# Performance work log

Hardware: AMD Instinct MI355X
Metric: run time of the kernel (lower is better)

Reference implementation:

```python
import jax, jax.numpy as jnp
import numpy as np

T_TASKS = 16      # num_tasks
N = 65536         # points per task (equal n per task -> r = 1 in the scatter)
NOISE = 100.0     # diagonal noise added at lag 0 of diagonal kernel blocks


def setup_inputs() -> dict:
    key = jax.random.key(0)
    k1_key, y_key = jax.random.split(key)
    # k1[i0, i1] : first row of the circulant kernel block for task pair (i0, i1)
    k1 = jax.random.normal(k1_key, (T_TASKS, T_TASKS, N), dtype=jnp.float32) * 0.01
    idx = jnp.arange(T_TASKS)
    k1 = k1.at[idx, idx, 0].add(NOISE)  # k1[0] += noise on diagonal blocks
    y = jax.random.normal(y_key, (T_TASKS, N), dtype=jnp.float32)
    return {"k1": k1, "y": y}


def _block_inverse(lams):
    """Sequential Schur-complement recursion from _InverseLogDetCache.

    lams: (T, T, N) complex eigenvalue vectors; only upper triangle (i0<=i1) used.
    Returns A: (T, T, N) complex (per-frequency inverse blocks), logdet (real scalar).
    """
    logdet = jnp.sum(jnp.log(jnp.abs(lams[0, 0])))
    A = (1.0 / lams[0, 0])[None, None, :]              # (1, 1, N)
    for l in range(1, lams.shape[0]):                   # loop over tasks (small, fixed)
        B = lams[:l, l, :]                              # (l, N)
        Tm = jnp.einsum('ikn,kn->in', A, B)             # T = A @ B per frequency
        M = jnp.sum(B.conj() * Tm, axis=0)              # (N,)
        S = lams[l, l] - M                              # Schur complement
        logdet = logdet + jnp.sum(jnp.log(jnp.abs(S)))
        Sinv = 1.0 / S
        P = Tm * Sinv                                   # (l, N)
        # C = P T^H + A  (r = 1 => meshgrid scatter is elementwise add of A)
        C = A + P[:, None, :] * Tm[None, :, :].conj()   # (l, l, N)
        ur = jnp.concatenate([C, -P[:, None, :]], axis=1)                     # (l, l+1, N)
        br = jnp.concatenate([-P.conj()[None, :, :], Sinv[None, None, :]], axis=1)  # (1, l+1, N)
        A = jnp.concatenate([ur, br], axis=0)           # (l+1, l+1, N)
    return A, logdet


def reference(k1, y):
    # lam = sqrt(n) * ortho-FFT(k1) == plain FFT(k1)
    lams = jnp.fft.fft(k1, axis=-1)                     # (T, T, N) complex64
    A, logdet = _block_inverse(lams)
    yt = jnp.fft.fft(y, axis=-1, norm='ortho')          # ytilde, (T, N) complex64
    quad = jnp.real(jnp.einsum('in,ijn,jn->', yt.conj(), A, yt))  # yt^H A yt
    out = jnp.concatenate([A.real.ravel(), A.imag.ravel(),
                           jnp.stack([logdet, quad]).astype(jnp.float32)])
    return out
```

## Files before the change

### kernel.cpp

```cpp
#include <hip/hip_runtime.h>
#include <hip/hip_fp16.h>


#define TT 16
#define NF 65536
#define NPAIR 136
#define NROWS 152
#define NHALF 32768

static const size_t AIMAG  = 16777216;
static const size_t OUT_LD = 33554432;
static const size_t OUT_QD = 33554433;

typedef float2 c32;

__device__ __forceinline__ c32 cmul(c32 a, c32 b) { return make_float2(a.x*b.x - a.y*b.y, a.x*b.y + a.y*b.x); }
__device__ __forceinline__ c32 cadd(c32 a, c32 b) { return make_float2(a.x + b.x, a.y + b.y); }
__device__ __forceinline__ c32 csub(c32 a, c32 b) { return make_float2(a.x - b.x, a.y - b.y); }

__constant__ c32 W16[16] = {
  { 1.0f, 0.0f}, { 0.92387953f,-0.38268343f}, { 0.70710678f,-0.70710678f}, { 0.38268343f,-0.92387953f},
  { 0.0f,-1.0f}, {-0.38268343f,-0.92387953f}, {-0.70710678f,-0.70710678f}, {-0.92387953f,-0.38268343f},
  {-1.0f, 0.0f}, {-0.92387953f, 0.38268343f}, {-0.70710678f, 0.70710678f}, {-0.38268343f, 0.92387953f},
  { 0.0f, 1.0f}, { 0.38268343f, 0.92387953f}, { 0.70710678f, 0.70710678f}, { 0.92387953f, 0.38268343f}
};

__device__ __forceinline__ void dft4(c32 a0, c32 a1, c32 a2, c32 a3,
                                     c32& c0, c32& c1, c32& c2, c32& c3) {
  c32 s0 = cadd(a0, a2), s1 = csub(a0, a2);
  c32 s2 = cadd(a1, a3), s3 = csub(a1, a3);
  c0 = cadd(s0, s2);
  c2 = csub(s0, s2);
  c1 = make_float2(s1.x + s3.y, s1.y - s3.x);
  c3 = make_float2(s1.x - s3.y, s1.y + s3.x);
}

__device__ __forceinline__ void dft16(c32 v[16]) {
  c32 t[16];
  #pragma unroll
  for (int p = 0; p < 4; ++p) {
    c32 c0, c1, c2, c3;
    dft4(v[p], v[p+4], v[p+8], v[p+12], c0, c1, c2, c3);
    t[4*p+0] = c0;
    t[4*p+1] = cmul(c1, W16[p]);
    t[4*p+2] = cmul(c2, W16[(2*p) & 15]);
    t[4*p+3] = cmul(c3, W16[(3*p) & 15]);
  }
  #pragma unroll
  for (int q = 0; q < 4; ++q) {
    c32 c0, c1, c2, c3;
    dft4(t[q], t[q+4], t[q+8], t[q+12], c0, c1, c2, c3);
    v[q+0]  = c0;
    v[q+4]  = c1;
    v[q+8]  = c2;
    v[q+12] = c3;
  }
}

__global__ __launch_bounds__(256) void fftA(const float* __restrict__ k1,
                                            const float* __restrict__ y,
                                            c32* __restrict__ out) {
  __shared__ c32 buf[16][258];
  const int t = threadIdx.x;
  const int c = t & 15;
  const int w = t >> 4;
  const int n2 = (blockIdx.x << 4) + c;
  const int row = blockIdx.y;
  const float* src;
  float scale = 1.0f;
  if (row < NPAIR) {
    int i = 0, rem = row;
    while (rem >= TT - i) { rem -= TT - i; ++i; }
    int j = i + rem;
    src = k1 + (size_t)(i * TT + j) * NF;
  } else {
    src = y + (size_t)(row - NPAIR) * NF;
    scale = 1.0f / 256.0f;
  }
  c32 v[16];
  #pragma unroll
  for (int i = 0; i < 16; ++i)
    v[i] = make_float2(src[(w + 16*i) * 256 + n2] * scale, 0.0f);
  dft16(v);
  {
    float sa, ca;
    __sincosf(-6.2831853071795865f * (float)w / 256.0f, &sa, &ca);
    c32 w1 = make_float2(ca, sa), wj = w1;
    #pragma unroll
    for (int j = 1; j < 16; ++j) { v[j] = cmul(v[j], wj); wj = cmul(wj, w1); }
  }
  #pragma unroll
  for (int j = 0; j < 16; ++j) buf[c][16*w + j] = v[j];
  __syncthreads();
  c32 u[16];
  #pragma unroll
  for (int i = 0; i < 16; ++i) u[i] = buf[c][w + 16*i];
  dft16(u);
  float sa, ca;
  __sincosf(-6.2831853071795865f * (float)(n2 * w) / 65536.0f, &sa, &ca);
  c32 tw = make_float2(ca, sa);
  __sincosf(-6.2831853071795865f * (float)n2 / 4096.0f, &sa, &ca);
  c32 st = make_float2(ca, sa);
  c32* dst = out + (size_t)row * NF + n2;
  #pragma unroll
  for (int j = 0; j < 16; ++j) {
    dst[(size_t)(w + 16*j) << 8] = cmul(u[j], tw);
    tw = cmul(tw, st);
  }
}

__global__ __launch_bounds__(256) void fftB(const c32* __restrict__ in,
                                            c32* __restrict__ out) {
  __shared__ c32 buf[16][258];
  const int t = threadIdx.x;
  const int c = t & 15;
  const int w = t >> 4;
  const int c0 = blockIdx.x << 4;
  const int row = blockIdx.y;
  const c32* src = in + (size_t)row * NF + ((size_t)c0 << 8);
  #pragma unroll
  for (int it = 0; it < 16; ++it) buf[it][t] = src[(it << 8) + t];
  __syncthreads();
  c32 v[16];
  #pragma unroll
  for (int i = 0; i < 16; ++i) v[i] = buf[c][w + 16*i];
  dft16(v);
  {
    float sa, ca;
    __sincosf(-6.2831853071795865f * (float)w / 256.0f, &sa, &ca);
    c32 w1 = make_float2(ca, sa), wj = w1;
    #pragma unroll
    for (int j = 1; j < 16; ++j) { v[j] = cmul(v[j], wj); wj = cmul(wj, w1); }
  }
  __syncthreads();
  #pragma unroll
  for (int j = 0; j < 16; ++j) buf[c][16*w + j] = v[j];
  __syncthreads();
  c32 u[16];
  #pragma unroll
  for (int i = 0; i < 16; ++i) u[i] = buf[c][w + 16*i];
  dft16(u);
  c32* dst = out + (size_t)row * NF + c0 + c;
  #pragma unroll
  for (int j = 0; j < 16; ++j) {
    int k2 = w + 16*j;
    if (k2 <= 128) dst[(size_t)k2 << 8] = u[j];
  }
}

__global__ void init_out(float* __restrict__ out) {
  if (threadIdx.x == 0 && blockIdx.x == 0) {
    out[OUT_LD] = 0.0f;
    out[OUT_QD] = 0.0f;
  }
}

__global__ __launch_bounds__(256) void invert_write(const c32* __restrict__ spec,
                                                    float* __restrict__ out) {
  __shared__ union {
    struct {
      __half2 lam[NPAIR][16];
      c32 yts[16][17];
      float4 tmb[16][17];
    } rec;
    float plane[16][260];
  } sh;
  __shared__ float redl[4], redq[4];

  const int nwg  = gridDim.x;
  const int orig = blockIdx.x;
  const int xcd  = orig & 7;
  const int pos  = orig >> 3;
  const int qq   = nwg >> 3, rm = nwg & 7;
  const int chunk = (xcd < rm ? xcd * (qq + 1) : rm * (qq + 1) + (xcd - rm) * qq) + pos;

  const int t  = threadIdx.x;
  const int fi = t >> 4;
  const int r  = t & 15;
  const int f0 = chunk << 4;
  const int f  = f0 + fi;

  for (int idx = t; idx < NPAIR * 16; idx += 256) {
    int rowi = idx >> 4, ff = idx & 15;
    c32 val = spec[(size_t)rowi * NF + f0 + ff];
    sh.rec.lam[rowi][ff] = __float22half2_rn(val);
  }
  for (int idx = NPAIR * 16 + t; idx < NROWS * 16; idx += 256) {
    int rowi = idx >> 4, ff = idx & 15;
    sh.rec.yts[ff][rowi - NPAIR] = spec[(size_t)rowi * NF + f0 + ff];
  }
  __syncthreads();

  const int rowoff = (r * (31 - r)) >> 1;

  float Ar[16], Ai[16];
  #pragma unroll
  for (int k = 0; k < 16; ++k) { Ar[k] = 0.0f; Ai[k] = 0.0f; }

  c32 l00 = __half22float2(sh.rec.lam[0][fi]);
  float m00 = l00.x*l00.x + l00.y*l00.y;
  float im00 = 1.0f / m00;
  float ld = 0.5f * __logf(m00);
  bool r0 = (r == 0);
  Ar[0] = r0 ?  l00.x * im00 : 0.0f;
  Ai[0] = r0 ? -l00.y * im00 : 0.0f;

  #pragma unroll
  for (int l = 1; l < TT; ++l) {
    float tr = 0.0f, ti = 0.0f;
    #pragma unroll
    for (int k = 0; k < l; ++k) {
      c32 B = __half22float2(sh.rec.lam[((k * (31 - k)) >> 1) + l][fi]);
      tr += Ar[k]*B.x - Ai[k]*B.y;
      ti += Ar[k]*B.y + Ai[k]*B.x;
    }
    c32 Bo = __half22float2(sh.rec.lam[rowoff + l][fi]);
    float cbr = Bo.x*tr + Bo.y*ti;
    float cbi = Bo.x*ti - Bo.y*tr;
    sh.rec.tmb[fi][r] = make_float4(tr, ti, cbr, cbi);

    float tjr[TT], tji[TT];
    float mr = 0.0f, mi = 0.0f;
    #pragma unroll
    for (int j = 0; j < l; ++j) {
      float4 q = sh.rec.tmb[fi][j];
      tjr[j] = q.x; tji[j] = q.y;
      mr += q.z;    mi += q.w;
    }

    c32 ll = __half22float2(sh.rec.lam[((l * (31 - l)) >> 1) + l][fi]);
    float Sr = ll.x - mr, Si = ll.y - mi;
    float s2 = Sr*Sr + Si*Si;
    ld += 0.5f * __logf(s2);
    float is2 = 1.0f / s2;
    float vr =  Sr * is2;
    float vi = -Si * is2;
    float pr = tr*vr - ti*vi;
    float pi = tr*vi + ti*vr;

    bool diag = (r == l);
    float cr = diag ? -vr : pr;
    float ci = diag ?  vi : pi;
    float m  = diag ? 0.0f : 1.0f;

    #pragma unroll
    for (int j = 0; j < l; ++j) {
      Ar[j] = m*Ar[j] + cr*tjr[j] + ci*tji[j];
      Ai[j] = m*Ai[j] + ci*tjr[j] - cr*tji[j];
    }
    Ar[l] = diag ? vr : -pr;
    Ai[l] = diag ? vi : -pi;
  }

  float w = (f == 0 || f == NHALF) ? 1.0f : (f < NHALF ? 2.0f : 0.0f);

  float sr = 0.0f, si = 0.0f;
  #pragma unroll
  for (int j = 0; j < 16; ++j) {
    c32 yj = sh.rec.yts[fi][j];
    sr += Ar[j]*yj.x - Ai[j]*yj.y;
    si += Ar[j]*yj.y + Ai[j]*yj.x;
  }
  c32 yr = sh.rec.yts[fi][r];
  float qd = (yr.x*sr + yr.y*si) * w;
  float lw = r0 ? ld * w : 0.0f;

  #pragma unroll
  for (int d = 1; d < 64; d <<= 1) {
    lw += __shfl_xor(lw, d, 64);
    qd += __shfl_xor(qd, d, 64);
  }
  if ((t & 63) == 0) { redl[t >> 6] = lw; redq[t >> 6] = qd; }
  __syncthreads();
  if (t == 0) {
    atomicAdd(out + OUT_LD, redl[0] + redl[1] + redl[2] + redl[3]);
    atomicAdd(out + OUT_QD, redq[0] + redq[1] + redq[2] + redq[3]);
  }

  const int lf = t & 15;
  const int cl = t >> 4;
  const int fL = f0 + lf;
  const bool dir_ok = (fL <= NHALF);
  const bool mir_ok = (fL > 0 && fL < NHALF);
  const size_t fD = (size_t)fL;
  const size_t fM = (size_t)(NF - fL);

  #pragma unroll
  for (int j = 0; j < 16; ++j) sh.plane[fi][r * 16 + ((j + r) & 15)] = Ar[j];
  __syncthreads();
  #pragma unroll
  for (int u = 0; u < 16; ++u) {
    int rr = u * 16 + cl;
    float v = sh.plane[lf][u * 16 + ((cl + u) & 15)];
    size_t o = (size_t)rr * NF;
    if (dir_ok) out[o + fD] = v;
    if (mir_ok) out[o + fM] = v;
  }
  __syncthreads();
  #pragma unroll
  for (int j = 0; j < 16; ++j) sh.plane[fi][r * 16 + ((j + r) & 15)] = Ai[j];
  __syncthreads();
  #pragma unroll
  for (int u = 0; u < 16; ++u) {
    int rr = u * 16 + cl;
    float v = sh.plane[lf][u * 16 + ((cl + u) & 15)];
    size_t o = AIMAG + (size_t)rr * NF;
    if (dir_ok) out[o + fD] = v;
    if (mir_ok) out[o + fM] = -v;
  }
}

extern "C" void kernel_launch(void* const* d_in, const int* in_sizes, int n_in,
                              void* d_out, int out_size, void* d_ws, size_t ws_size,
                              hipStream_t stream) {
  const float* k1 = (const float*)d_in[0];
  const float* y  = (const float*)d_in[1];
  float* out = (float*)d_out;
  c32* spec1 = (c32*)d_out;
  c32* spec  = (c32*)d_ws;

  dim3 grid(16, NROWS);
  dim3 blk(256);

  fftA<<<grid, blk, 0, stream>>>(k1, y, spec1);
  fftB<<<grid, blk, 0, stream>>>(spec1, spec);

  init_out<<<1, 64, 0, stream>>>(out);
  invert_write<<<2049, blk, 0, stream>>>(spec, out);
}
```

Measured before the change: 142.0 us.

## Relayout half-precision lambda shared memory for vectorized column loads, use nontemporal stores

The shared-memory eigenvalue array is reorganized from pair-major [pair][freq] to frequency-major per-column groups padded to 4-element chunks. Each thread can then fetch a whole column of B values with a few 128-bit LDS reads instead of many scalar loads. The output A-plane stores are switched to nontemporal stores to avoid polluting cache with write-only data. The fill loop gains a small per-element while loop to compute the new index, and the new layout may change LDS bank conflicts.

New measurement: 167.7 us. +18.1%, slower.

```diff
diff --git a/kernel.cpp b/kernel.cpp
--- a/kernel.cpp
+++ b/kernel.cpp
@@ -17,6 +17,12 @@
 __device__ __forceinline__ c32 cmul(c32 a, c32 b) { return make_float2(a.x*b.x - a.y*b.y, a.x*b.y + a.y*b.x); }
 __device__ __forceinline__ c32 cadd(c32 a, c32 b) { return make_float2(a.x + b.x, a.y + b.y); }
 __device__ __forceinline__ c32 csub(c32 a, c32 b) { return make_float2(a.x - b.x, a.y - b.y); }
+
+__host__ __device__ constexpr int colbase(int l) {
+  int g = l >> 2;
+  return 8 * g * (g + 1) + (l & 3) * 4 * (g + 1);
+}
+#define LAMW 168
 
 __constant__ c32 W16[16] = {
   { 1.0f, 0.0f}, { 0.92387953f,-0.38268343f}, { 0.70710678f,-0.70710678f}, { 0.38268343f,-0.92387953f},
@@ -155,11 +161,16 @@
   }
 }
 
+__device__ __forceinline__ c32 h2f(unsigned int u) {
+  __half2 h = *(__half2*)&u;
+  return __half22float2(h);
+}
+
 __global__ __launch_bounds__(256) void invert_write(const c32* __restrict__ spec,
                                                     float* __restrict__ out) {
   __shared__ union {
     struct {
-      __half2 lam[NPAIR][16];
+      __half2 lam2[16][LAMW];
       c32 yts[16][17];
       float4 tmb[16][17];
     } rec;
@@ -181,9 +192,13 @@
   const int f  = f0 + fi;
 
   for (int idx = t; idx < NPAIR * 16; idx += 256) {
-    int rowi = idx >> 4, ff = idx & 15;
-    c32 val = spec[(size_t)rowi * NF + f0 + ff];
-    sh.rec.lam[rowi][ff] = __float22half2_rn(val);
+    int e = idx >> 4, ff = idx & 15;
+    int i = 0, rem = e;
+    while (rem >= TT - i) { rem -= TT - i; ++i; }
+    int j = i + rem;
+    int g = j >> 2;
+    int d = 8 * g * (g + 1) + (j & 3) * 4 * (g + 1) + i;
+    sh.rec.lam2[ff][d] = __float22half2_rn(spec[(size_t)e * NF + f0 + ff]);
   }
   for (int idx = NPAIR * 16 + t; idx < NROWS * 16; idx += 256) {
     int rowi = idx >> 4, ff = idx & 15;
@@ -191,13 +206,13 @@
   }
   __syncthreads();
 
-  const int rowoff = (r * (31 - r)) >> 1;
+  const __half2* lamrow = &sh.rec.lam2[fi][0];
 
   float Ar[16], Ai[16];
   #pragma unroll
   for (int k = 0; k < 16; ++k) { Ar[k] = 0.0f; Ai[k] = 0.0f; }
 
-  c32 l00 = __half22float2(sh.rec.lam[0][fi]);
+  c32 l00 = h2f(*(const unsigned int*)&lamrow[0]);
   float m00 = l00.x*l00.x + l00.y*l00.y;
   float im00 = 1.0f / m00;
   float ld = 0.5f * __logf(m00);
@@ -207,14 +222,25 @@
 
   #pragma unroll
   for (int l = 1; l < TT; ++l) {
+    const int sl = colbase(l);
+    unsigned int chw[16];
+    #pragma unroll
+    for (int cc = 0; cc < 4; ++cc) {
+      if (cc * 4 <= l) {
+        uint4 raw = *(const uint4*)&lamrow[sl + 4*cc];
+        chw[4*cc+0] = raw.x; chw[4*cc+1] = raw.y;
+        chw[4*cc+2] = raw.z; chw[4*cc+3] = raw.w;
+      }
+    }
     float tr = 0.0f, ti = 0.0f;
     #pragma unroll
     for (int k = 0; k < l; ++k) {
-      c32 B = __half22float2(sh.rec.lam[((k * (31 - k)) >> 1) + l][fi]);
+      c32 B = h2f(chw[k]);
       tr += Ar[k]*B.x - Ai[k]*B.y;
       ti += Ar[k]*B.y + Ai[k]*B.x;
     }
-    c32 Bo = __half22float2(sh.rec.lam[rowoff + l][fi]);
+    int kk = (r <= l) ? r : 0;
+    c32 Bo = h2f(*(const unsigned int*)&lamrow[sl + kk]);
     float cbr = Bo.x*tr + Bo.y*ti;
     float cbi = Bo.x*ti - Bo.y*tr;
     sh.rec.tmb[fi][r] = make_float4(tr, ti, cbr, cbi);
@@ -228,7 +254,7 @@
       mr += q.z;    mi += q.w;
     }
 
-    c32 ll = __half22float2(sh.rec.lam[((l * (31 - l)) >> 1) + l][fi]);
+    c32 ll = h2f(chw[l]);
     float Sr = ll.x - mr, Si = ll.y - mi;
     float s2 = Sr*Sr + Si*Si;
     ld += 0.5f * __logf(s2);
@@ -293,8 +319,8 @@
     int rr = u * 16 + cl;
     float v = sh.plane[lf][u * 16 + ((cl + u) & 15)];
     size_t o = (size_t)rr * NF;
-    if (dir_ok) out[o + fD] = v;
-    if (mir_ok) out[o + fM] = v;
+    if (dir_ok) __builtin_nontemporal_store(v, &out[o + fD]);
+    if (mir_ok) __builtin_nontemporal_store(v, &out[o + fM]);
   }
   __syncthreads();
   #pragma unroll
@@ -305,8 +331,8 @@
     int rr = u * 16 + cl;
     float v = sh.plane[lf][u * 16 + ((cl + u) & 15)];
     size_t o = AIMAG + (size_t)rr * NF;
-    if (dir_ok) out[o + fD] = v;
-    if (mir_ok) out[o + fM] = -v;
+    if (dir_ok) __builtin_nontemporal_store(v, &out[o + fD]);
+    if (mir_ok) __builtin_nontemporal_store(-v, &out[o + fM]);
   }
 }
 
```
